# Kernel optimization log

Measured on AMD Instinct MI355X. Metric: run time of the kernel, lower is better.

The kernel has to match this reference:

```python
import jax, jax.numpy as jnp
import numpy as np

EPS = 1e-6

def setup_inputs() -> dict:
    key = jax.random.key(0)
    k1, k2, k3 = jax.random.split(key, 3)
    B, L, H, D = 8, 4096, 8, 64
    queries = jax.random.normal(k1, (B, L, H, D), dtype=jnp.float32)
    keys = jax.random.normal(k2, (B, L, H, D), dtype=jnp.float32)
    values = jax.random.normal(k3, (B, L, H, D), dtype=jnp.float32)
    return {"queries": queries, "keys": keys, "values": values, "attn_mask": 0}


def reference(queries, keys, values, attn_mask):
    # [B, L, H, D] -> [B, H, L, D]
    q = jnp.transpose(queries, (0, 2, 1, 3))
    k = jnp.transpose(keys, (0, 2, 1, 3))
    v = jnp.transpose(values, (0, 2, 1, 3))
    # sigmoid kernel feature map
    q = jax.nn.sigmoid(q)
    k = jax.nn.sigmoid(k)
    L = q.shape[2]
    S = k.shape[2]
    # stage-1 normalizers
    normalizer_row = 1.0 / jnp.einsum('nhld,nhd->nhl', q + EPS, k.sum(axis=2) + EPS)  # [B,H,L]
    normalizer_col = 1.0 / jnp.einsum('nhsd,nhd->nhs', k + EPS, q.sum(axis=2) + EPS)  # [B,H,S]
    # stage-2 refined normalizers
    nr_refine = jnp.einsum('nhld,nhd->nhl', q + EPS,
                           (k * normalizer_col[..., None]).sum(axis=2) + EPS)
    nc_refine = jnp.einsum('nhsd,nhd->nhs', k + EPS,
                           (q * normalizer_row[..., None]).sum(axis=2) + EPS)
    nr_refine = jax.nn.sigmoid(nr_refine * (float(L) / float(S)))
    nc_refine = jax.nn.softmax(nc_refine, axis=-1) * S
    # linear attention: kv = K^T @ (V * col_refine)
    kv = jnp.einsum('nhsd,nhse->nhde', k, v * nc_refine[..., None])  # [B,H,D,D]
    x = jnp.einsum('nhld,nhde->nhle', q, kv) * normalizer_row[..., None] * nr_refine[..., None]
    # back to [B, L, H, D]
    return jnp.transpose(x, (0, 2, 1, 3))
```

## Files before the change

kernel.cpp:

```cpp
#include <hip/hip_runtime.h>

#define EPSF 1e-6f

#define NB 8
#define LL 4096
#define NHD 8
#define DD 64
#define ROWSTR 512
#define NSTR (LL * ROWSTR)

#define OFF_QSUM 0
#define OFF_KSUM 4096
#define OFF_QNSUM 8192
#define OFF_KNSUM 12288
#define OFF_KV 16448
#define OFF_KVP (OFF_KV + 262144)
#define KVP_FLOATS (64 * 16 * 4096)
#define OFF_KP1 OFF_KVP
#define OFF_QP1 (OFF_KVP + 1048576)
#define OFF_QNP1 (OFF_KVP + 2097152)
#define OFF_KNP (OFF_KVP + KVP_FLOATS)
#define OFF_ZP (OFF_KNP + 65536)

typedef __attribute__((ext_vector_type(8))) short short8v;
typedef __attribute__((ext_vector_type(4))) float f32x4;

__device__ __forceinline__ float sigf(float x) {
  return 1.0f / (1.0f + __expf(-x));
}

__device__ __forceinline__ float rsum16(float p) {
  p += __shfl_xor(p, 1, 16);
  p += __shfl_xor(p, 2, 16);
  p += __shfl_xor(p, 4, 16);
  p += __shfl_xor(p, 8, 16);
  return p;
}

__device__ __forceinline__ float rsum8(float p) {
  p += __shfl_xor(p, 1, 8);
  p += __shfl_xor(p, 2, 8);
  p += __shfl_xor(p, 4, 8);
  return p;
}

__device__ __forceinline__ unsigned short b16rne(float x) {
  unsigned int u = __float_as_uint(x);
  return (unsigned short)((u + 0x7FFFu + ((u >> 16) & 1u)) >> 16);
}

__device__ __forceinline__ unsigned int pack2(float a, float b) {
  return (unsigned int)b16rne(a) | ((unsigned int)b16rne(b) << 16);
}

__global__ __launch_bounds__(256) void k_ksum(const float* __restrict__ k,
                                              float* __restrict__ ws) {
  int bid = blockIdx.x;
  int n = bid >> 8, chunk = bid & 255;
  int t = threadIdx.x;
  const float* base = k + (size_t)n * NSTR + (size_t)chunk * 16 * ROWSTR + t * 4;
  float4 acc = make_float4(0.f, 0.f, 0.f, 0.f);
#pragma unroll
  for (int it = 0; it < 8; ++it) {
    const float4 x = *(const float4*)(base + (size_t)it * 1024);
    acc.x += sigf(x.x); acc.y += sigf(x.y); acc.z += sigf(x.z); acc.w += sigf(x.w);
  }
  __shared__ float red[512];
  if (t < 128) {
    red[t * 4 + 0] = acc.x; red[t * 4 + 1] = acc.y;
    red[t * 4 + 2] = acc.z; red[t * 4 + 3] = acc.w;
  }
  __syncthreads();
  if (t >= 128) {
    int c = (t - 128) * 4;
    red[c + 0] += acc.x; red[c + 1] += acc.y;
    red[c + 2] += acc.z; red[c + 3] += acc.w;
  }
  __syncthreads();
  if (t < 128)
    *(float4*)(ws + OFF_KP1 + (size_t)bid * 512 + t * 4) = *(float4*)&red[t * 4];
}

__global__ __launch_bounds__(256) void k_red1(const float* __restrict__ src,
                                              float* __restrict__ dst) {
  int bid = blockIdx.x;
  int n = bid >> 3, cg = bid & 7;
  int t = threadIdx.x;
  int col = cg * 64 + (t & 63);
  int ci = t >> 6;
  const float* base = src + (size_t)n * 256 * 512 + col;
  float s = 0.f;
#pragma unroll 8
  for (int c = 0; c < 64; ++c) s += base[(size_t)(ci * 64 + c) * 512];
  __shared__ float red[4][64];
  red[ci][t & 63] = s;
  __syncthreads();
  if (t < 64)
    dst[n * 512 + cg * 64 + t] = red[0][t] + red[1][t] + red[2][t] + red[3][t];
}

__global__ __launch_bounds__(256) void k_qpass(const float* __restrict__ q,
                                               float* __restrict__ ws) {
  int bid = blockIdx.x;
  int n = bid >> 8, chunk = bid & 255;
  int t = threadIdx.x;
  int col = (t * 4) & 511;
  __shared__ float vec[512];
  if (t < 128) {
    const float* kp = ws + OFF_KSUM + n * 512 + t * 4;
    vec[t * 4 + 0] = kp[0] + EPSF; vec[t * 4 + 1] = kp[1] + EPSF;
    vec[t * 4 + 2] = kp[2] + EPSF; vec[t * 4 + 3] = kp[3] + EPSF;
  }
  __syncthreads();
  const float4 ve = *(const float4*)&vec[col];
  const float* base = q + (size_t)n * NSTR + (size_t)chunk * 16 * ROWSTR + t * 4;
  float4 qacc = make_float4(0.f, 0.f, 0.f, 0.f);
  float4 nacc = make_float4(0.f, 0.f, 0.f, 0.f);
#pragma unroll
  for (int it = 0; it < 8; ++it) {
    const float4 x = *(const float4*)(base + (size_t)it * 1024);
    float4 s;
    s.x = sigf(x.x); s.y = sigf(x.y); s.z = sigf(x.z); s.w = sigf(x.w);
    qacc.x += s.x; qacc.y += s.y; qacc.z += s.z; qacc.w += s.w;
    float p = (s.x + EPSF) * ve.x + (s.y + EPSF) * ve.y +
              (s.z + EPSF) * ve.z + (s.w + EPSF) * ve.w;
    p = rsum16(p);
    float nrm = 1.0f / p;
    nacc.x += s.x * nrm; nacc.y += s.y * nrm; nacc.z += s.z * nrm; nacc.w += s.w * nrm;
  }
  __shared__ float red[512];
  if (t < 128) {
    red[t * 4 + 0] = qacc.x; red[t * 4 + 1] = qacc.y;
    red[t * 4 + 2] = qacc.z; red[t * 4 + 3] = qacc.w;
  }
  __syncthreads();
  if (t >= 128) {
    int c = (t - 128) * 4;
    red[c + 0] += qacc.x; red[c + 1] += qacc.y;
    red[c + 2] += qacc.z; red[c + 3] += qacc.w;
  }
  __syncthreads();
  if (t < 128)
    *(float4*)(ws + OFF_QP1 + (size_t)bid * 512 + t * 4) = *(float4*)&red[t * 4];
  __syncthreads();
  if (t < 128) {
    red[t * 4 + 0] = nacc.x; red[t * 4 + 1] = nacc.y;
    red[t * 4 + 2] = nacc.z; red[t * 4 + 3] = nacc.w;
  }
  __syncthreads();
  if (t >= 128) {
    int c = (t - 128) * 4;
    red[c + 0] += nacc.x; red[c + 1] += nacc.y;
    red[c + 2] += nacc.z; red[c + 3] += nacc.w;
  }
  __syncthreads();
  if (t < 128)
    *(float4*)(ws + OFF_QNP1 + (size_t)bid * 512 + t * 4) = *(float4*)&red[t * 4];
}

__global__ __launch_bounds__(256) void k_redq(float* __restrict__ ws) {
  int bid = blockIdx.x;
  int which = bid >> 6, id = bid & 63;
  const float* src = ws + (which ? OFF_QNP1 : OFF_QP1);
  float* dst = ws + (which ? OFF_QNSUM : OFF_QSUM);
  int n = id >> 3, cg = id & 7;
  int t = threadIdx.x;
  int col = cg * 64 + (t & 63);
  int ci = t >> 6;
  const float* base = src + (size_t)n * 256 * 512 + col;
  float s = 0.f;
#pragma unroll 8
  for (int c = 0; c < 64; ++c) s += base[(size_t)(ci * 64 + c) * 512];
  __shared__ float red[4][64];
  red[ci][t & 63] = s;
  __syncthreads();
  if (t < 64)
    dst[n * 512 + cg * 64 + t] = red[0][t] + red[1][t] + red[2][t] + red[3][t];
}

__global__ __launch_bounds__(512, 4) void k_kv(const float* __restrict__ k,
                                               const float* __restrict__ v,
                                               float* __restrict__ ws) {
  const int bid = blockIdx.x;
  const int nh = bid >> 4, chunk = bid & 15;
  const int n = nh >> 3, h = nh & 7;
  const int t = threadIdx.x;

  __shared__ unsigned short kt[64][72];
  __shared__ unsigned short vt[64][72];
  __shared__ float knred[8][64];
  __shared__ float zw[8];

  const float* kbase = k + (size_t)n * NSTR + h * DD;
  const float* vbase = v + (size_t)n * NSTR + h * DD;

  const int srow_l = t >> 3;
  const int tq = t & 7;
  const int c0 = tq * 4, c1 = 32 + tq * 4;
  const int s0 = chunk * 256;

  const float* qnp = ws + OFF_QNSUM + nh * 64;
  float4 qa = *(const float4*)(qnp + c0);
  float4 qb = *(const float4*)(qnp + c1);
  qa.x += EPSF; qa.y += EPSF; qa.z += EPSF; qa.w += EPSF;
  qb.x += EPSF; qb.y += EPSF; qb.z += EPSF; qb.w += EPSF;
  const float* qsp = ws + OFF_QSUM + nh * 64;
  float4 sa = *(const float4*)(qsp + c0);
  float4 sb = *(const float4*)(qsp + c1);
  sa.x += EPSF; sa.y += EPSF; sa.z += EPSF; sa.w += EPSF;
  sb.x += EPSF; sb.y += EPSF; sb.z += EPSF; sb.w += EPSF;

  const int w = t >> 6, lane = t & 63;
  const int dblk = w >> 1, ep = w & 1;
  const int m = lane & 15, grp = lane >> 4;
  const int arow = 16 * dblk + m;
  const int brow0 = 16 * (2 * ep) + m;
  const int brow1 = 16 * (2 * ep + 1) + m;

  f32x4 acc0 = {0.f, 0.f, 0.f, 0.f};
  f32x4 acc1 = {0.f, 0.f, 0.f, 0.f};
  float zloc = 0.f;
  float knacc[8];
#pragma unroll
  for (int i = 0; i < 8; ++i) knacc[i] = 0.f;

  const float* krow = kbase + (size_t)(s0 + srow_l) * ROWSTR;
  const float* vrow = vbase + (size_t)(s0 + srow_l) * ROWSTR;
  float4 kA = *(const float4*)(krow + c0);
  float4 kB = *(const float4*)(krow + c1);
  float4 vA = *(const float4*)(vrow + c0);
  float4 vB = *(const float4*)(vrow + c1);

  for (int sub = 0; sub < 4; ++sub) {
    float4 kAn, kBn, vAn, vBn;
    if (sub < 3) {
      const float* krn = kbase + (size_t)(s0 + (sub + 1) * 64 + srow_l) * ROWSTR;
      const float* vrn = vbase + (size_t)(s0 + (sub + 1) * 64 + srow_l) * ROWSTR;
      kAn = *(const float4*)(krn + c0);
      kBn = *(const float4*)(krn + c1);
      vAn = *(const float4*)(vrn + c0);
      vBn = *(const float4*)(vrn + c1);
    }
    float sk[8];
    sk[0] = sigf(kA.x); sk[1] = sigf(kA.y); sk[2] = sigf(kA.z); sk[3] = sigf(kA.w);
    sk[4] = sigf(kB.x); sk[5] = sigf(kB.y); sk[6] = sigf(kB.z); sk[7] = sigf(kB.w);
    float p = (sk[0] + EPSF) * qa.x + (sk[1] + EPSF) * qa.y +
              (sk[2] + EPSF) * qa.z + (sk[3] + EPSF) * qa.w +
              (sk[4] + EPSF) * qb.x + (sk[5] + EPSF) * qb.y +
              (sk[6] + EPSF) * qb.z + (sk[7] + EPSF) * qb.w;
    float p2 = (sk[0] + EPSF) * sa.x + (sk[1] + EPSF) * sa.y +
               (sk[2] + EPSF) * sa.z + (sk[3] + EPSF) * sa.w +
               (sk[4] + EPSF) * sb.x + (sk[5] + EPSF) * sb.y +
               (sk[6] + EPSF) * sb.z + (sk[7] + EPSF) * sb.w;
    p = rsum8(p);
    p2 = rsum8(p2);
    float wgt = __expf(p);
    if (tq == 0) zloc += wgt;
    float inv2 = 1.0f / p2;
#pragma unroll
    for (int i = 0; i < 8; ++i) knacc[i] += sk[i] * inv2;
    float vv[8] = {vA.x, vA.y, vA.z, vA.w, vB.x, vB.y, vB.z, vB.w};
#pragma unroll
    for (int i = 0; i < 8; ++i) {
      int d = (i < 4) ? (c0 + i) : (c1 + i - 4);
      kt[d][srow_l] = b16rne(sk[i] * wgt);
      vt[d][srow_l] = b16rne(vv[i]);
    }
    __syncthreads();
#pragma unroll
    for (int ks = 0; ks < 2; ++ks) {
      const int sb2 = ks * 32 + 8 * grp;
      short8v A  = *(const short8v*)&kt[arow][sb2];
      short8v B0 = *(const short8v*)&vt[brow0][sb2];
      short8v B1 = *(const short8v*)&vt[brow1][sb2];
      acc0 = __builtin_amdgcn_mfma_f32_16x16x32_bf16(A, B0, acc0, 0, 0, 0);
      acc1 = __builtin_amdgcn_mfma_f32_16x16x32_bf16(A, B1, acc1, 0, 0, 0);
    }
    __syncthreads();
    kA = kAn; kB = kBn; vA = vAn; vB = vBn;
  }

  float* dst = ws + OFF_KVP + (size_t)bid * 4096;
  const int drow = 16 * dblk + 4 * grp;
#pragma unroll
  for (int r = 0; r < 4; ++r) {
    dst[(drow + r) * 64 + brow0] = acc0[r];
    dst[(drow + r) * 64 + brow1] = acc1[r];
  }

#pragma unroll
  for (int i = 0; i < 8; ++i) {
    knacc[i] += __shfl_xor(knacc[i], 8, 64);
    knacc[i] += __shfl_xor(knacc[i], 16, 64);
    knacc[i] += __shfl_xor(knacc[i], 32, 64);
  }
  if (lane < 8) {
#pragma unroll
    for (int i = 0; i < 4; ++i) {
      knred[w][lane * 4 + i] = knacc[i];
      knred[w][32 + lane * 4 + i] = knacc[4 + i];
    }
  }
  zloc += __shfl_xor(zloc, 8, 64);
  zloc += __shfl_xor(zloc, 16, 64);
  zloc += __shfl_xor(zloc, 32, 64);
  if (lane == 0) zw[w] = zloc;
  __syncthreads();
  if (t < 64) {
    float s = 0.f;
#pragma unroll
    for (int ww = 0; ww < 8; ++ww) s += knred[ww][t];
    ws[OFF_KNP + (size_t)bid * 64 + t] = s;
  }
  if (t == 0) {
    float s = 0.f;
#pragma unroll
    for (int ww = 0; ww < 8; ++ww) s += zw[ww];
    ws[OFF_ZP + bid] = s;
  }
}

__global__ __launch_bounds__(256) void k_kvred(float* __restrict__ ws) {
  int nh = blockIdx.x;
  int t = threadIdx.x;
  const float* zp = ws + OFF_ZP;
  float z = 0.f;
#pragma unroll
  for (int c = 0; c < 16; ++c) z += zp[nh * 16 + c];
  float scale = (float)LL / z;
  if (t < 64) {
    const float* knp = ws + OFF_KNP;
    float s = 0.f;
#pragma unroll
    for (int c = 0; c < 16; ++c) s += knp[(size_t)(nh * 16 + c) * 64 + t];
    ws[OFF_KNSUM + nh * 64 + t] = s;
  }
  __shared__ float lds[64][69];
  const float4* src = (const float4*)(ws + OFF_KVP);
#pragma unroll
  for (int i = 0; i < 4; ++i) {
    int off = i * 256 + t;
    float4 s = make_float4(0.f, 0.f, 0.f, 0.f);
#pragma unroll
    for (int c = 0; c < 16; ++c) {
      float4 x = src[(size_t)((nh * 16 + c) << 10) + off];
      s.x += x.x; s.y += x.y; s.z += x.z; s.w += x.w;
    }
    int d = off >> 4, e0 = (off & 15) * 4;
    lds[d][e0 + 0] = s.x * scale; lds[d][e0 + 1] = s.y * scale;
    lds[d][e0 + 2] = s.z * scale; lds[d][e0 + 3] = s.w * scale;
  }
  __syncthreads();
  int e = t >> 2, d0 = (t & 3) * 16;
  unsigned int words[8];
#pragma unroll
  for (int j = 0; j < 8; ++j)
    words[j] = pack2(lds[d0 + 2 * j][e], lds[d0 + 2 * j + 1][e]);
  unsigned int* dstp = (unsigned int*)((unsigned short*)(ws + OFF_KV) + (size_t)nh * 4096 + e * 64 + d0);
#pragma unroll
  for (int j = 0; j < 8; ++j) dstp[j] = words[j];
}

__global__ __launch_bounds__(256) void k_out(const float* __restrict__ q,
                                             float* __restrict__ out,
                                             const float* __restrict__ ws) {
  int bid = blockIdx.x;
  int nh = bid >> 5, chunk = bid & 31;
  int n = nh >> 3, h = nh & 7;
  int t = threadIdx.x, tq = t & 15, g = t >> 4;
  __shared__ unsigned short sqb[128][72];
  __shared__ unsigned short kvb[64][72];
  __shared__ float scl[128];
  __shared__ float ksv[64], knv[64];
  if (t < 64) {
    ksv[t] = ws[OFF_KSUM + nh * 64 + t] + EPSF;
    knv[t] = ws[OFF_KNSUM + nh * 64 + t] + EPSF;
  }
  {
    int r0 = t >> 2, c0 = (t & 3) * 16;
    const short8v* gsrc = (const short8v*)((const unsigned short*)(ws + OFF_KV) +
                                           (size_t)nh * 4096 + r0 * 64 + c0);
    short8v a = gsrc[0], b = gsrc[1];
    *(short8v*)&kvb[r0][c0] = a;
    *(short8v*)&kvb[r0][c0 + 8] = b;
  }
  __syncthreads();
  const float4 ke = *(const float4*)&ksv[tq * 4];
  const float4 kne = *(const float4*)&knv[tq * 4];
  const float* qbase = q + (size_t)n * NSTR + h * DD + tq * 4;
  int l0 = chunk * 128;
#pragma unroll
  for (int rr = 0; rr < 8; ++rr) {
    int row = g + rr * 16;
    const float4 x = *(const float4*)(qbase + (size_t)(l0 + row) * ROWSTR);
    float4 s;
    s.x = sigf(x.x); s.y = sigf(x.y); s.z = sigf(x.z); s.w = sigf(x.w);
    *(unsigned int*)&sqb[row][tq * 4] = pack2(s.x, s.y);
    *(unsigned int*)&sqb[row][tq * 4 + 2] = pack2(s.z, s.w);
    float p1 = (s.x + EPSF) * ke.x + (s.y + EPSF) * ke.y +
               (s.z + EPSF) * ke.z + (s.w + EPSF) * ke.w;
    float p2 = (s.x + EPSF) * kne.x + (s.y + EPSF) * kne.y +
               (s.z + EPSF) * kne.z + (s.w + EPSF) * kne.w;
    p1 = rsum16(p1);
    p2 = rsum16(p2);
    if (tq == 0) scl[row] = (1.0f / p1) * sigf(p2);
  }
  __syncthreads();
  int w = t >> 6, lane = t & 63;
  int m = lane & 15, grp = lane >> 4;
  f32x4 a00 = {0,0,0,0}, a01 = {0,0,0,0}, a02 = {0,0,0,0}, a03 = {0,0,0,0};
  f32x4 a10 = {0,0,0,0}, a11 = {0,0,0,0}, a12 = {0,0,0,0}, a13 = {0,0,0,0};
#pragma unroll
  for (int ks = 0; ks < 2; ++ks) {
    const int sb = ks * 32 + 8 * grp;
    short8v A0 = *(const short8v*)&sqb[(2 * w + 0) * 16 + m][sb];
    short8v A1 = *(const short8v*)&sqb[(2 * w + 1) * 16 + m][sb];
    short8v B0 = *(const short8v*)&kvb[0 * 16 + m][sb];
    short8v B1 = *(const short8v*)&kvb[1 * 16 + m][sb];
    short8v B2 = *(const short8v*)&kvb[2 * 16 + m][sb];
    short8v B3 = *(const short8v*)&kvb[3 * 16 + m][sb];
    a00 = __builtin_amdgcn_mfma_f32_16x16x32_bf16(A0, B0, a00, 0, 0, 0);
    a01 = __builtin_amdgcn_mfma_f32_16x16x32_bf16(A0, B1, a01, 0, 0, 0);
    a02 = __builtin_amdgcn_mfma_f32_16x16x32_bf16(A0, B2, a02, 0, 0, 0);
    a03 = __builtin_amdgcn_mfma_f32_16x16x32_bf16(A0, B3, a03, 0, 0, 0);
    a10 = __builtin_amdgcn_mfma_f32_16x16x32_bf16(A1, B0, a10, 0, 0, 0);
    a11 = __builtin_amdgcn_mfma_f32_16x16x32_bf16(A1, B1, a11, 0, 0, 0);
    a12 = __builtin_amdgcn_mfma_f32_16x16x32_bf16(A1, B2, a12, 0, 0, 0);
    a13 = __builtin_amdgcn_mfma_f32_16x16x32_bf16(A1, B3, a13, 0, 0, 0);
  }
  float* obase = out + (size_t)n * NSTR + h * DD;
#pragma unroll
  for (int mt = 0; mt < 2; ++mt) {
    int lrow = (2 * w + mt) * 16 + 4 * grp;
#pragma unroll
    for (int r = 0; r < 4; ++r) {
      float sc = scl[lrow + r];
      float* orow = obase + (size_t)(l0 + lrow + r) * ROWSTR;
      if (mt == 0) {
        orow[0 * 16 + m] = a00[r] * sc; orow[1 * 16 + m] = a01[r] * sc;
        orow[2 * 16 + m] = a02[r] * sc; orow[3 * 16 + m] = a03[r] * sc;
      } else {
        orow[0 * 16 + m] = a10[r] * sc; orow[1 * 16 + m] = a11[r] * sc;
        orow[2 * 16 + m] = a12[r] * sc; orow[3 * 16 + m] = a13[r] * sc;
      }
    }
  }
}

extern "C" void kernel_launch(void* const* d_in, const int* in_sizes, int n_in,
                              void* d_out, int out_size, void* d_ws, size_t ws_size,
                              hipStream_t stream) {
  const float* q = (const float*)d_in[0];
  const float* k = (const float*)d_in[1];
  const float* v = (const float*)d_in[2];
  float* out = (float*)d_out;
  float* ws = (float*)d_ws;

  hipLaunchKernelGGL(k_ksum, dim3(2048), dim3(256), 0, stream, k, ws);
  hipLaunchKernelGGL(k_red1, dim3(64), dim3(256), 0, stream, ws + OFF_KP1, ws + OFF_KSUM);
  hipLaunchKernelGGL(k_qpass, dim3(2048), dim3(256), 0, stream, q, ws);
  hipLaunchKernelGGL(k_redq, dim3(128), dim3(256), 0, stream, ws);
  hipLaunchKernelGGL(k_kv, dim3(1024), dim3(512), 0, stream, k, v, ws);
  hipLaunchKernelGGL(k_kvred, dim3(64), dim3(256), 0, stream, ws);
  hipLaunchKernelGGL(k_out, dim3(2048), dim3(256), 0, stream, q, out, ws);
}
```

Before: 104.6 us.

## Split k_kv into smaller 256-thread blocks and store KV partials as bf16

The K^T·V partial-product kernel now runs 2048 blocks of 256 threads, each covering 128 sequence rows instead of 256. Each wave owns a 16-row D block across all four 16-column output tiles, and the shared tiles shrink to one 32-row slice. The per-block 64x64 partials are written as bf16 instead of fp32, and the reducer sums 32 bf16 partials per head. This cuts partial-buffer traffic and raises occupancy, at the cost of extra bf16 rounding before the final sum and twice as many partials to reduce.

```diff
diff --git a/kernel.cpp b/kernel.cpp
--- a/kernel.cpp
+++ b/kernel.cpp
@@ -20,7 +20,7 @@
 #define OFF_QP1 (OFF_KVP + 1048576)
 #define OFF_QNP1 (OFF_KVP + 2097152)
 #define OFF_KNP (OFF_KVP + KVP_FLOATS)
-#define OFF_ZP (OFF_KNP + 65536)
+#define OFF_ZP (OFF_KNP + 131072)
 
 typedef __attribute__((ext_vector_type(8))) short short8v;
 typedef __attribute__((ext_vector_type(4))) float f32x4;
@@ -51,6 +51,10 @@
 
 __device__ __forceinline__ unsigned int pack2(float a, float b) {
   return (unsigned int)b16rne(a) | ((unsigned int)b16rne(b) << 16);
+}
+
+__device__ __forceinline__ float bf2f(unsigned short u) {
+  return __uint_as_float(((unsigned int)u) << 16);
 }
 
 __global__ __launch_bounds__(256) void k_ksum(const float* __restrict__ k,
@@ -178,18 +182,17 @@
     dst[n * 512 + cg * 64 + t] = red[0][t] + red[1][t] + red[2][t] + red[3][t];
 }
 
-__global__ __launch_bounds__(512, 4) void k_kv(const float* __restrict__ k,
+__global__ __launch_bounds__(256, 8) void k_kv(const float* __restrict__ k,
                                                const float* __restrict__ v,
                                                float* __restrict__ ws) {
   const int bid = blockIdx.x;
-  const int nh = bid >> 4, chunk = bid & 15;
+  const int nh = bid >> 5, chunk = bid & 31;
   const int n = nh >> 3, h = nh & 7;
   const int t = threadIdx.x;
 
-  __shared__ unsigned short kt[64][72];
-  __shared__ unsigned short vt[64][72];
-  __shared__ float knred[8][64];
-  __shared__ float zw[8];
+  __shared__ unsigned short smem[2][64][40];
+  float* knred = (float*)&smem[0][0][0];
+  float* zw = knred + 256;
 
   const float* kbase = k + (size_t)n * NSTR + h * DD;
   const float* vbase = v + (size_t)n * NSTR + h * DD;
@@ -197,7 +200,7 @@
   const int srow_l = t >> 3;
   const int tq = t & 7;
   const int c0 = tq * 4, c1 = 32 + tq * 4;
-  const int s0 = chunk * 256;
+  const int s0 = chunk * 128;
 
   const float* qnp = ws + OFF_QNSUM + nh * 64;
   float4 qa = *(const float4*)(qnp + c0);
@@ -211,14 +214,13 @@
   sb.x += EPSF; sb.y += EPSF; sb.z += EPSF; sb.w += EPSF;
 
   const int w = t >> 6, lane = t & 63;
-  const int dblk = w >> 1, ep = w & 1;
   const int m = lane & 15, grp = lane >> 4;
-  const int arow = 16 * dblk + m;
-  const int brow0 = 16 * (2 * ep) + m;
-  const int brow1 = 16 * (2 * ep + 1) + m;
-
-  f32x4 acc0 = {0.f, 0.f, 0.f, 0.f};
-  f32x4 acc1 = {0.f, 0.f, 0.f, 0.f};
+  const int arow = w * 16 + m;
+  const int sbr = 8 * grp;
+
+  f32x4 acc[4];
+#pragma unroll
+  for (int j = 0; j < 4; ++j) acc[j] = (f32x4){0.f, 0.f, 0.f, 0.f};
   float zloc = 0.f;
   float knacc[8];
 #pragma unroll
@@ -234,8 +236,8 @@
   for (int sub = 0; sub < 4; ++sub) {
     float4 kAn, kBn, vAn, vBn;
     if (sub < 3) {
-      const float* krn = kbase + (size_t)(s0 + (sub + 1) * 64 + srow_l) * ROWSTR;
-      const float* vrn = vbase + (size_t)(s0 + (sub + 1) * 64 + srow_l) * ROWSTR;
+      const float* krn = kbase + (size_t)(s0 + (sub + 1) * 32 + srow_l) * ROWSTR;
+      const float* vrn = vbase + (size_t)(s0 + (sub + 1) * 32 + srow_l) * ROWSTR;
       kAn = *(const float4*)(krn + c0);
       kBn = *(const float4*)(krn + c1);
       vAn = *(const float4*)(vrn + c0);
@@ -263,30 +265,29 @@
 #pragma unroll
     for (int i = 0; i < 8; ++i) {
       int d = (i < 4) ? (c0 + i) : (c1 + i - 4);
-      kt[d][srow_l] = b16rne(sk[i] * wgt);
-      vt[d][srow_l] = b16rne(vv[i]);
+      smem[0][d][srow_l] = b16rne(sk[i] * wgt);
+      smem[1][d][srow_l] = b16rne(vv[i]);
     }
     __syncthreads();
-#pragma unroll
-    for (int ks = 0; ks < 2; ++ks) {
-      const int sb2 = ks * 32 + 8 * grp;
-      short8v A  = *(const short8v*)&kt[arow][sb2];
-      short8v B0 = *(const short8v*)&vt[brow0][sb2];
-      short8v B1 = *(const short8v*)&vt[brow1][sb2];
-      acc0 = __builtin_amdgcn_mfma_f32_16x16x32_bf16(A, B0, acc0, 0, 0, 0);
-      acc1 = __builtin_amdgcn_mfma_f32_16x16x32_bf16(A, B1, acc1, 0, 0, 0);
+    {
+      short8v A = *(const short8v*)&smem[0][arow][sbr];
+#pragma unroll
+      for (int j = 0; j < 4; ++j) {
+        short8v B = *(const short8v*)&smem[1][j * 16 + m][sbr];
+        acc[j] = __builtin_amdgcn_mfma_f32_16x16x32_bf16(A, B, acc[j], 0, 0, 0);
+      }
     }
     __syncthreads();
     kA = kAn; kB = kBn; vA = vAn; vB = vBn;
   }
 
-  float* dst = ws + OFF_KVP + (size_t)bid * 4096;
-  const int drow = 16 * dblk + 4 * grp;
-#pragma unroll
-  for (int r = 0; r < 4; ++r) {
-    dst[(drow + r) * 64 + brow0] = acc0[r];
-    dst[(drow + r) * 64 + brow1] = acc1[r];
-  }
+  unsigned short* dst = (unsigned short*)(ws + OFF_KVP) + (size_t)bid * 4096;
+  const int drow = w * 16 + 4 * grp;
+#pragma unroll
+  for (int j = 0; j < 4; ++j)
+#pragma unroll
+    for (int r = 0; r < 4; ++r)
+      dst[(drow + r) * 64 + j * 16 + m] = b16rne(acc[j][r]);
 
 #pragma unroll
   for (int i = 0; i < 8; ++i) {
@@ -294,30 +295,23 @@
     knacc[i] += __shfl_xor(knacc[i], 16, 64);
     knacc[i] += __shfl_xor(knacc[i], 32, 64);
   }
-  if (lane < 8) {
-#pragma unroll
-    for (int i = 0; i < 4; ++i) {
-      knred[w][lane * 4 + i] = knacc[i];
-      knred[w][32 + lane * 4 + i] = knacc[4 + i];
-    }
-  }
   zloc += __shfl_xor(zloc, 8, 64);
   zloc += __shfl_xor(zloc, 16, 64);
   zloc += __shfl_xor(zloc, 32, 64);
+  if (lane < 8) {
+#pragma unroll
+    for (int i = 0; i < 4; ++i) {
+      knred[w * 64 + lane * 4 + i] = knacc[i];
+      knred[w * 64 + 32 + lane * 4 + i] = knacc[4 + i];
+    }
+  }
   if (lane == 0) zw[w] = zloc;
   __syncthreads();
   if (t < 64) {
-    float s = 0.f;
-#pragma unroll
-    for (int ww = 0; ww < 8; ++ww) s += knred[ww][t];
+    float s = knred[t] + knred[64 + t] + knred[128 + t] + knred[192 + t];
     ws[OFF_KNP + (size_t)bid * 64 + t] = s;
   }
-  if (t == 0) {
-    float s = 0.f;
-#pragma unroll
-    for (int ww = 0; ww < 8; ++ww) s += zw[ww];
-    ws[OFF_ZP + bid] = s;
-  }
+  if (t == 0) ws[OFF_ZP + bid] = zw[0] + zw[1] + zw[2] + zw[3];
 }
 
 __global__ __launch_bounds__(256) void k_kvred(float* __restrict__ ws) {
@@ -326,29 +320,35 @@
   const float* zp = ws + OFF_ZP;
   float z = 0.f;
 #pragma unroll
-  for (int c = 0; c < 16; ++c) z += zp[nh * 16 + c];
+  for (int c = 0; c < 32; ++c) z += zp[nh * 32 + c];
   float scale = (float)LL / z;
   if (t < 64) {
     const float* knp = ws + OFF_KNP;
     float s = 0.f;
 #pragma unroll
-    for (int c = 0; c < 16; ++c) s += knp[(size_t)(nh * 16 + c) * 64 + t];
+    for (int c = 0; c < 32; ++c) s += knp[(size_t)(nh * 32 + c) * 64 + t];
     ws[OFF_KNSUM + nh * 64 + t] = s;
   }
+  float accv[16];
+#pragma unroll
+  for (int j = 0; j < 16; ++j) accv[j] = 0.f;
+  const unsigned short* src = (const unsigned short*)(ws + OFF_KVP);
+#pragma unroll 4
+  for (int c = 0; c < 32; ++c) {
+    const unsigned short* base = src + (size_t)(nh * 32 + c) * 4096 + t * 16;
+    short8v a = *(const short8v*)base;
+    short8v b = *(const short8v*)(base + 8);
+#pragma unroll
+    for (int j = 0; j < 8; ++j) {
+      accv[j] += bf2f((unsigned short)a[j]);
+      accv[8 + j] += bf2f((unsigned short)b[j]);
+    }
+  }
   __shared__ float lds[64][69];
-  const float4* src = (const float4*)(ws + OFF_KVP);
-#pragma unroll
-  for (int i = 0; i < 4; ++i) {
-    int off = i * 256 + t;
-    float4 s = make_float4(0.f, 0.f, 0.f, 0.f);
-#pragma unroll
-    for (int c = 0; c < 16; ++c) {
-      float4 x = src[(size_t)((nh * 16 + c) << 10) + off];
-      s.x += x.x; s.y += x.y; s.z += x.z; s.w += x.w;
-    }
-    int d = off >> 4, e0 = (off & 15) * 4;
-    lds[d][e0 + 0] = s.x * scale; lds[d][e0 + 1] = s.y * scale;
-    lds[d][e0 + 2] = s.z * scale; lds[d][e0 + 3] = s.w * scale;
+  {
+    int d = t >> 2, e0 = (t & 3) * 16;
+#pragma unroll
+    for (int j = 0; j < 16; ++j) lds[d][e0 + j] = accv[j] * scale;
   }
   __syncthreads();
   int e = t >> 2, d0 = (t & 3) * 16;
@@ -460,7 +460,7 @@
   hipLaunchKernelGGL(k_red1, dim3(64), dim3(256), 0, stream, ws + OFF_KP1, ws + OFF_KSUM);
   hipLaunchKernelGGL(k_qpass, dim3(2048), dim3(256), 0, stream, q, ws);
   hipLaunchKernelGGL(k_redq, dim3(128), dim3(256), 0, stream, ws);
-  hipLaunchKernelGGL(k_kv, dim3(1024), dim3(512), 0, stream, k, v, ws);
+  hipLaunchKernelGGL(k_kv, dim3(2048), dim3(256), 0, stream, k, v, ws);
   hipLaunchKernelGGL(k_kvred, dim3(64), dim3(256), 0, stream, ws);
   hipLaunchKernelGGL(k_out, dim3(2048), dim3(256), 0, stream, q, out, ws);
 }
```

Result: slower. 165.5 us (+58.2%).
